# Optimization experiments

Measured on AMD Instinct MI355X. Metric: run time of the kernel, lower is better.

Reference implementation:

```python
import jax, jax.numpy as jnp
import numpy as np
from jax import lax

K = 8          # num_classes
C_IN = 256     # in_channels
EPS = 1e-5


def resize_bilinear_ac(x, H, W):
    """Bilinear resize with align_corners=True. x: [B,C,h,w] -> [B,C,H,W]."""
    B, C, h, w = x.shape
    if h == H and w == W:
        return x
    ys = jnp.linspace(0.0, h - 1.0, H)
    xs = jnp.linspace(0.0, w - 1.0, W)
    y0 = jnp.floor(ys).astype(jnp.int32)
    x0 = jnp.floor(xs).astype(jnp.int32)
    y1 = jnp.minimum(y0 + 1, h - 1)
    x1 = jnp.minimum(x0 + 1, w - 1)
    wy = (ys - y0.astype(x.dtype))[None, None, :, None]
    wx = (xs - x0.astype(x.dtype))[None, None, None, :]
    g00 = x[:, :, y0][:, :, :, x0]
    g01 = x[:, :, y0][:, :, :, x1]
    g10 = x[:, :, y1][:, :, :, x0]
    g11 = x[:, :, y1][:, :, :, x1]
    top = g00 * (1.0 - wx) + g01 * wx
    bot = g10 * (1.0 - wx) + g11 * wx
    return top * (1.0 - wy) + bot * wy


def setup_inputs() -> dict:
    key = jax.random.key(0)
    ks = jax.random.split(key, 16)
    shapes = [(2, 256, 128, 128), (2, 256, 64, 64), (2, 256, 32, 32), (2, 256, 16, 16), (2, 256, 8, 8)]
    inp = {}
    for i, s in enumerate(shapes):
        inp[f"feat{i}"] = jax.random.normal(ks[i], s, dtype=jnp.float32)
    inp["attr_feat"] = jax.random.normal(ks[5], (2, K * C_IN, 64, 64), dtype=jnp.float32)
    # learned params
    inp["mlp_f_w"] = jax.random.normal(ks[6], (256, 256), dtype=jnp.float32) * 0.02
    inp["mlp_f_b"] = jnp.zeros((256,), dtype=jnp.float32)
    inp["mlp_a_w"] = jax.random.normal(ks[7], (256, 256), dtype=jnp.float32) * 0.02
    inp["mlp_a_b"] = jnp.zeros((256,), dtype=jnp.float32)
    # 5 grouped convs: [out=2048, in_per_group=256, 3, 3] each, no bias (BN follows)
    inp["conv_w"] = jax.random.normal(ks[8], (5, K * C_IN, C_IN, 3, 3), dtype=jnp.float32) * 0.02
    inp["bn_gamma"] = jnp.ones((5, K * C_IN), dtype=jnp.float32)
    inp["bn_beta"] = jnp.zeros((5, K * C_IN), dtype=jnp.float32)
    inp["bn_mean"] = jax.random.normal(ks[9], (5, K * C_IN), dtype=jnp.float32) * 0.1
    inp["bn_var"] = jax.random.uniform(ks[10], (5, K * C_IN), dtype=jnp.float32, minval=0.5, maxval=1.5)
    return inp


def _forward(feats, attr_feat, mlp_f_w, mlp_f_b, mlp_a_w, mlp_a_b, conv_w, bn_gamma, bn_beta, bn_mean, bn_var):
    B = attr_feat.shape[0]
    # global avg pool attr -> [B, K, C] -> mlp_a
    avg_attr = attr_feat.mean(axis=(2, 3)).reshape(B, K, C_IN)
    avg_attr = avg_attr @ mlp_a_w.T + mlp_a_b  # [B,K,256]
    outs = []
    for i, x in enumerate(feats):
        _, C, H, W = x.shape
        avg_x = x.mean(axis=(2, 3)) @ mlp_f_w.T + mlp_f_b          # [B,256]
        logits = jnp.einsum('bkc,bc->bk', avg_attr, avg_x)          # [B,K]
        attn = jax.nn.softmax(logits, axis=-1)
        y = resize_bilinear_ac(attr_feat, H, W)                      # [B,2048,H,W]
        y = lax.conv_general_dilated(
            y, conv_w[i], window_strides=(1, 1), padding=((1, 1), (1, 1)),
            dimension_numbers=('NCHW', 'OIHW', 'NCHW'), feature_group_count=K)
        inv = lax.rsqrt(bn_var[i] + EPS)
        y = (y - bn_mean[i][None, :, None, None]) * (inv * bn_gamma[i])[None, :, None, None] + bn_beta[i][None, :, None, None]
        y = jax.nn.relu(y)
        y = y.reshape(B, K, C, H, W)
        y = jnp.einsum('bkchw,bk->bchw', y, attn)                   # weighted sum over classes
        outs.append(jax.nn.relu(x + y))
    return tuple(outs)


def reference(feat0, feat1, feat2, feat3, feat4, attr_feat, mlp_f_w, mlp_f_b, mlp_a_w, mlp_a_b, conv_w, bn_gamma, bn_beta, bn_mean, bn_var):
    feats = [feat0, feat1, feat2, feat3, feat4]
    return _forward(feats, attr_feat, mlp_f_w, mlp_f_b, mlp_a_w, mlp_a_b, conv_w, bn_gamma, bn_beta, bn_mean, bn_var)
```

## Files before the change

kernel.cpp:

```cpp
#include <hip/hip_runtime.h>
#include <hip/hip_bf16.h>
#include <cstdint>

typedef __attribute__((ext_vector_type(8))) short short8;
typedef __attribute__((ext_vector_type(4))) float f32x4;

#define EPSV 1e-5f

__device__ __forceinline__ void gload_lds16(const void* g, void* l) {
  __builtin_amdgcn_global_load_lds(
      (const __attribute__((address_space(1))) void*)(uintptr_t)g,
      (__attribute__((address_space(3))) void*)(uint32_t)(uintptr_t)l,
      16, 0, 0);
}

__device__ __forceinline__ uint32_t f2bf_rne(float v) {
  const uint32_t u = __float_as_uint(v);
  const uint32_t r = ((u >> 16) & 1u) + 0x7fffu;
  return (u + r) >> 16;
}

__global__ void mean_kernel(const float* __restrict__ in, float* __restrict__ out,
                            int HW, float inv) {
  const int ch = blockIdx.x;
  const int t = threadIdx.x;
  const float* p = in + (size_t)ch * HW;
  float s = 0.f;
  const int nv = HW >> 2;
  const float4* pv = (const float4*)p;
  for (int i = t; i < nv; i += 256) { float4 v = pv[i]; s += v.x + v.y + v.z + v.w; }
  __shared__ float red[256];
  red[t] = s; __syncthreads();
  for (int off = 128; off > 0; off >>= 1) {
    if (t < off) red[t] += red[t + off];
    __syncthreads();
  }
  if (t == 0) out[ch] = red[0] * inv;
}

__global__ void wtrans_kernel(const float* __restrict__ cw,
                              const float* __restrict__ gamma, const float* __restrict__ beta,
                              const float* __restrict__ mean, const float* __restrict__ var,
                              __hip_bfloat16* __restrict__ wt, float* __restrict__ bias) {
  const int oc = blockIdx.x;
  const int i  = blockIdx.y;
  const int ci = threadIdx.x;
  const int idx = i * 2048 + oc;
  const float sc = rsqrtf(var[idx] + EPSV) * gamma[idx];
  if (ci == 0) bias[idx] = beta[idx] - mean[idx] * sc;
  const int g = oc >> 8, co = oc & 255;
  const float* src = cw + ((size_t)idx * 256 + ci) * 9;
  const size_t dbase = (size_t)(i * 8 + g) * 9 * 65536 + co * 256 + ci;
#pragma unroll
  for (int tap = 0; tap < 9; ++tap)
    wt[dbase + (size_t)tap * 65536] = __float2bfloat16(src[tap] * sc);
}

__global__ void gate_kernel(const float* __restrict__ meanA, const float* __restrict__ meanF,
                            const float* __restrict__ Wa, const float* __restrict__ ba,
                            const float* __restrict__ Wf, const float* __restrict__ bfp,
                            float* __restrict__ attn) {
  __shared__ float mA[16 * 256];
  __shared__ float mF[10 * 256];
  __shared__ float pA[16 * 256];
  __shared__ float pF[10 * 256];
  __shared__ float lg[80];
// ... 70 lines not shown
  const int cc = t >> 2, seg = (t & 3) * 16;
  const int bb = bk >> 3, k = bk & 7;
  const float* ab = attr + (size_t)bb * 2048 * 4096;
  const int ci = t & 63;
  for (int cq = 0; cq < 4; ++cq) {
    __syncthreads();
    {
      const int ch = k * 256 + cq * 64 + cc;
      const float* r0 = ab + ((size_t)ch * 64 + y0) * 64;
      const float* r1 = ab + ((size_t)ch * 64 + y1) * 64;
#pragma unroll
      for (int u = 0; u < 4; ++u) {
        float4 v0 = ((const float4*)r0)[(t & 3) * 4 + u];
        float4 v1 = ((const float4*)r1)[(t & 3) * 4 + u];
        buf[0][cc][seg + u * 4 + 0] = v0.x; buf[0][cc][seg + u * 4 + 1] = v0.y;
        buf[0][cc][seg + u * 4 + 2] = v0.z; buf[0][cc][seg + u * 4 + 3] = v0.w;
        buf[1][cc][seg + u * 4 + 0] = v1.x; buf[1][cc][seg + u * 4 + 1] = v1.y;
        buf[1][cc][seg + u * 4 + 2] = v1.z; buf[1][cc][seg + u * 4 + 3] = v1.w;
      }
    }
    __syncthreads();
    for (int x = t >> 6; x < W; x += 4) {
      const float fx = x * scl;
      int x0 = (int)floorf(fx); if (x0 > 63) x0 = 63;
      const float wx = fx - (float)x0;
      const int x1 = min(x0 + 1, 63);
      const float top = buf[0][ci][x0] * (1.f - wx) + buf[0][ci][x1] * wx;
      const float bot = buf[1][ci][x0] * (1.f - wx) + buf[1][ci][x1] * wx;
      R[rowbase + (size_t)(x + 1) * 256 + cq * 64 + ci] = __float2bfloat16(top * (1.f - wy) + bot * wy);
    }
    if (t < 64) {
      R[rowbase + cq * 64 + t] = __float2bfloat16(0.f);
      R[rowbase + (size_t)(Wp - 1) * 256 + cq * 64 + t] = __float2bfloat16(0.f);
    }
  }
}

__device__ __forceinline__ void coords36(int u, int g0, int& g, int& ty, int& tx, int& cq) {
  g = g0 + u / 36;
  const int r = u % 36;
  const int tap = r >> 2;
  cq = r & 3;
  ty = tap / 3;
  tx = tap - ty * 3;
}

__global__ __launch_bounds__(512, 1)
void conv256_kernel(const __hip_bfloat16* __restrict__ R,
                    const __hip_bfloat16* __restrict__ Wt,
                    const float* __restrict__ bias,
                    const float* __restrict__ attn,
                    __hip_bfloat16* __restrict__ zout,
                    int W, int lw, int Hp, int Wp, int HW,
                    int NB, int gcount) {
  __shared__ alignas(16) __hip_bfloat16 ldsA[2][256 * 64];
  __shared__ alignas(16) __hip_bfloat16 ldsB[2][256 * 64];
  const int tid  = threadIdx.x;
  const int lane = tid & 63;
  const int wave = __builtin_amdgcn_readfirstlane(tid >> 6);
  const int wm = (wave >> 2) * 128;
  const int wn = (wave & 3) * 64;

  const int nx  = gridDim.x;
  const int lin = blockIdx.x;
  const int pos = ((nx & 7) == 0) ? ((lin & 7) * (nx >> 3) + (lin >> 3)) : lin;
  const int n0  = pos * 256;

  const int bb = (int)blockIdx.y % NB;
  const int gs = (int)blockIdx.y / NB;
  const int g0 = gs * gcount;

  const int c8 = lane & 7, r8 = lane >> 3;
  const int sc = (c8 ^ r8) << 3;
  const int aoff0 = ((wave * 32 + r8) << 8) + sc;
  const int dst0  = wave * 2048;
  int boff[4];
#pragma unroll
  for (int q = 0; q < 4; ++q) {
    const int row = wave * 32 + q * 8 + r8;
    const int sg = n0 + row;
    const int y = sg >> lw, x = sg & (W - 1);
    boff[q] = ((y * Wp + x) << 8) + sc;
  }

  const size_t rgstride = (size_t)Hp * Wp * 256;
  const __hip_bfloat16* Rb = R + (size_t)bb * 8 * rgstride;

  const f32x4 fz = {0.f, 0.f, 0.f, 0.f};
  f32x4 acc[8][4];
  uint32_t finp[8][4][2];
#pragma unroll
  for (int mf = 0; mf < 8; ++mf)
#pragma unroll
    for (int nf = 0; nf < 4; ++nf) {
      acc[mf][nf] = fz; finp[mf][nf][0] = 0u; finp[mf][nf][1] = 0u;
    }

  const int nk = gcount * 36;
  {
    const __hip_bfloat16* wp = Wt + ((size_t)g0 * 9 << 16);
    const __hip_bfloat16* rp = Rb + (size_t)g0 * rgstride;
#pragma unroll
    for (int q = 0; q < 4; ++q) gload_lds16(wp + aoff0 + q * 2048, &ldsA[0][dst0 + q * 512]);
#pragma unroll
    for (int q = 0; q < 4; ++q) gload_lds16(rp + boff[q], &ldsB[0][dst0 + q * 512]);
  }

  int foldc = 0, gcur = g0;
  for (int t = 0; t < nk; ++t) {
    const int c = t & 1;
    const bool pf = (t + 1 < nk);
    int g1, ty1, tx1, cq1;
    coords36(pf ? t + 1 : t, g0, g1, ty1, tx1, cq1);
    const __hip_bfloat16* wp1 = Wt + (((size_t)g1 * 9 + ty1 * 3 + tx1) << 16) + (cq1 << 6);
    const __hip_bfloat16* rp1 = Rb + (size_t)g1 * rgstride + ((ty1 * Wp + tx1) << 8) + (cq1 << 6);

    asm volatile("s_waitcnt vmcnt(0)" ::: "memory");
    __builtin_amdgcn_s_barrier();
    asm volatile("" ::: "memory");

    const __hip_bfloat16* pA = &ldsA[c][0];
    const __hip_bfloat16* pB = &ldsB[c][0];
    __hip_bfloat16* dA = &ldsA[c ^ 1][0];
    __hip_bfloat16* dB = &ldsB[c ^ 1][0];

#pragma unroll
    for (int ks = 0; ks < 2; ++ks) {
      const int cb = ks * 4 + (lane >> 4);
      short8 bfv[4];
#pragma unroll
      for (int nf = 0; nf < 4; ++nf) {
        const int row = wn + nf * 16 + (lane & 15);
        bfv[nf] = *(const short8*)&pB[(row << 6) + ((cb ^ (row & 7)) << 3)];
      }
#pragma unroll
      for (int h = 0; h < 2; ++h) {
        short8 af[4];
#pragma unroll
        for (int m = 0; m < 4; ++m) {
          const int row = wm + (h * 4 + m) * 16 + (lane & 15);
          af[m] = *(const short8*)&pA[(row << 6) + ((cb ^ (row & 7)) << 3)];
        }
        if (ks == 0 && pf) {
          if (h == 0) {
#pragma unroll
            for (int q = 0; q < 4; ++q) gload_lds16(wp1 + aoff0 + q * 2048, dA + dst0 + q * 512);
          } else {
#pragma unroll
            for (int q = 0; q < 4; ++q) gload_lds16(rp1 + boff[q], dB + dst0 + q * 512);
          }
        }
        __builtin_amdgcn_s_barrier();
        __builtin_amdgcn_sched_barrier(0);
        __builtin_amdgcn_s_setprio(1);
#pragma unroll
        for (int m = 0; m < 4; ++m)
#pragma unroll
          for (int nf = 0; nf < 4; ++nf)
            acc[h * 4 + m][nf] = __builtin_amdgcn_mfma_f32_16x16x32_bf16(
                af[m], bfv[nf], acc[h * 4 + m][nf], 0, 0, 0);
        __builtin_amdgcn_s_setprio(0);
        __builtin_amdgcn_s_barrier();
        asm volatile("" ::: "memory");
      }
    }

    if (++foldc == 36) {
      foldc = 0;
      const float aw = attn[bb * 8 + gcur];
#pragma unroll
      for (int mf = 0; mf < 8; ++mf) {
        const int cobase = wm + mf * 16 + ((lane >> 4) << 2);
#pragma unroll
        for (int pr = 0; pr < 2; ++pr) {
          const float b0v = bias[(gcur << 8) + cobase + pr * 2 + 0];
          const float b1v = bias[(gcur << 8) + cobase + pr * 2 + 1];
#pragma unroll
          for (int nf = 0; nf < 4; ++nf) {
            const uint32_t p = finp[mf][nf][pr];
            const float f0 = __uint_as_float(p << 16)
                           + aw * fmaxf(acc[mf][nf][pr * 2 + 0] + b0v, 0.f);
            const float f1 = __uint_as_float(p & 0xffff0000u)
                           + aw * fmaxf(acc[mf][nf][pr * 2 + 1] + b1v, 0.f);
            finp[mf][nf][pr] = (f2bf_rne(f1) << 16) | f2bf_rne(f0);
          }
        }
#pragma unroll
        for (int nf = 0; nf < 4; ++nf) acc[mf][nf] = fz;
      }
      ++gcur;
    }
  }

  __hip_bfloat16* zb = zout + (size_t)(gs * 2 + bb) * 256 * (size_t)HW;
#pragma unroll
  for (int mf = 0; mf < 8; ++mf) {
    const int cobase = wm + mf * 16 + ((lane >> 4) << 2);
#pragma unroll
    for (int nf = 0; nf < 4; ++nf) {
      const int n = n0 + wn + nf * 16 + (lane & 15);
#pragma unroll
      for (int pr = 0; pr < 2; ++pr) {
        const uint32_t p = finp[mf][nf][pr];
        zb[(size_t)(cobase + pr * 2 + 0) * HW + n] =
            __float2bfloat16(__uint_as_float(p << 16));
        zb[(size_t)(cobase + pr * 2 + 1) * HW + n] =
            __float2bfloat16(__uint_as_float(p & 0xffff0000u));
      }
    }
  }
}

__global__ __launch_bounds__(256, 2)
void conv_kernel(const __hip_bfloat16* __restrict__ R,
                 const __hip_bfloat16* __restrict__ Wt,
                 const float* __restrict__ bias,
                 const float* __restrict__ attn,
                 const float* __restrict__ featp,
                 void* __restrict__ outp,
                 int W, int lw, int Hp, int Wp, int HW,
                 int b0, int NB, int gcount) {
  __shared__ alignas(16) __hip_bfloat16 ldsA[2][128 * 64];
  __shared__ alignas(16) __hip_bfloat16 ldsB[3][128 * 64];
  const int tid  = threadIdx.x;
  const int lane = tid & 63;
  const int wave = __builtin_amdgcn_readfirstlane(tid >> 6);
  const int wm = (wave >> 1) * 64;
  const int wn = (wave & 1) * 64;

  const int nx  = gridDim.x;
  const int lin = blockIdx.x;
  const int pos = ((nx & 7) == 0) ? ((lin & 7) * (nx >> 3) + (lin >> 3)) : lin;
  const int co0 = (pos & 1) * 128;
  const int n0  = (pos >> 1) * 128;

  const int bb  = (int)blockIdx.y % NB;
  const int gs  = (int)blockIdx.y / NB;
  const int b   = b0 + bb;
  const int g0  = gs * gcount;

  const int c8 = lane & 7;
  const int r8 = lane >> 3;
  int aoff[4], boff[4], dst[4];
#pragma unroll
  for (int q = 0; q < 4; ++q) {
    const int row = (wave * 4 + q) * 8 + r8;
    const int sc = (c8 ^ (row & 7)) << 3;
    aoff[q] = ((co0 + row) << 8) + sc;
    int sg = n0 + row; if (sg >= HW) sg = HW - 1;
    const int y = sg >> lw, x = sg & (W - 1);
    boff[q] = ((y * Wp + x) << 8) + sc;
    dst[q] = (wave * 4 + q) * 512;
  }

  const size_t rgstride = (size_t)Hp * Wp * 256;
  const __hip_bfloat16* Rb = R + (size_t)bb * 8 * rgstride;

  const f32x4 fz = {0.f, 0.f, 0.f, 0.f};
  f32x4 fin[4][4], acc[4][4];
#pragma unroll
// ... 122 lines not shown
        if (n < HW) {
#pragma unroll
          for (int r = 0; r < 4; ++r)
            zb[(size_t)(cobase + r) * HW + n] = __float2bfloat16(fin[mf][nf][r]);
        }
      }
    }
  }
}

__global__ void reduce_kernel(const __hip_bfloat16* __restrict__ z,
                              const float* __restrict__ feat,
                              float* __restrict__ outp, int total, int S) {
  const int i4 = (blockIdx.x * 256 + threadIdx.x) * 4;
  if (i4 >= total) return;
  float4 f = *(const float4*)(feat + i4);
  float s0 = f.x, s1 = f.y, s2 = f.z, s3 = f.w;
  for (int j = 0; j < S; ++j) {
    const ushort4 v = *(const ushort4*)(z + (size_t)j * total + i4);
    s0 += __uint_as_float((uint32_t)v.x << 16);
    s1 += __uint_as_float((uint32_t)v.y << 16);
    s2 += __uint_as_float((uint32_t)v.z << 16);
    s3 += __uint_as_float((uint32_t)v.w << 16);
  }
  float4 o = {fmaxf(s0, 0.f), fmaxf(s1, 0.f), fmaxf(s2, 0.f), fmaxf(s3, 0.f)};
  *(float4*)(outp + i4) = o;
}

extern "C" void kernel_launch(void* const* d_in, const int* in_sizes, int n_in,
                              void* d_out, int out_size, void* d_ws, size_t ws_size,
                              hipStream_t stream) {
  const float* feat[5];
  for (int i = 0; i < 5; ++i) feat[i] = (const float*)d_in[i];
  const float* attr = (const float*)d_in[5];
  const float* mfw = (const float*)d_in[6];
  const float* mfb = (const float*)d_in[7];
  const float* maw = (const float*)d_in[8];
  const float* mab = (const float*)d_in[9];
  const float* cw  = (const float*)d_in[10];
  const float* bng = (const float*)d_in[11];
  const float* bnb = (const float*)d_in[12];
  const float* bnm = (const float*)d_in[13];
  const float* bnv = (const float*)d_in[14];
  float* out = (float*)d_out;

  char* ws = (char*)d_ws;
  float* attnW = (float*)(ws);
  float* meanA = (float*)(ws + 512);
  float* meanF = (float*)(ws + 20480);
  float* biasW = (float*)(ws + 32768);
  __hip_bfloat16* Wt = (__hip_bfloat16*)(ws + 131072);
  const size_t R_OFF = 47316992;
  __hip_bfloat16* Rbuf = (__hip_bfloat16*)(ws + R_OFF);

  const bool full = ws_size >= (size_t)219316224;
  const int NB = full ? 2 : 1;
  __hip_bfloat16* zbuf = (__hip_bfloat16*)(ws + R_OFF + (size_t)NB * 69222400);

  static const int HS[5] = {128, 64, 32, 16, 8};
  static const size_t OOFF[5] = {0, 8388608, 10485760, 11010048, 11141120};

  mean_kernel<<<4096, 256, 0, stream>>>(attr, meanA, 4096, 1.f / 4096.f);
  for (int i = 0; i < 5; ++i) {
    const int HW = HS[i] * HS[i];
    mean_kernel<<<512, 256, 0, stream>>>(feat[i], meanF + i * 512, HW, 1.f / (float)HW);
  }
  wtrans_kernel<<<dim3(2048, 5), 256, 0, stream>>>(cw, bng, bnb, bnm, bnv, Wt, biasW);
  gate_kernel<<<1, 256, 0, stream>>>(meanA, meanF, maw, mab, mfw, mfb, attnW);

  for (int i = 0; i < 5; ++i) {
    const int H = HS[i], W = H, HW = H * W, Hp = H + 2, Wp = W + 2;
    const int lw = 31 - __builtin_clz((unsigned)W);
    const float scl = 63.f / (float)(H - 1);

    if (full) {
      resize_kernel<<<dim3(16, Hp), 256, 0, stream>>>(attr, Rbuf, W, Hp, Wp, scl);
      if (i <= 1) {
        const int S = (i == 0) ? 2 : 8;
        const int gcount = 8 / S;
        conv256_kernel<<<dim3(HW / 256, 2 * S), 512, 0, stream>>>(
            Rbuf, Wt + (size_t)i * 8 * 9 * 65536, biasW + i * 2048, attnW + i * 16,
            zbuf, W, lw, Hp, Wp, HW, 2, gcount);
        const int total = 2 * 256 * HW;
        reduce_kernel<<<(total / 4 + 255) / 256, 256, 0, stream>>>(
            zbuf, feat[i], out + OOFF[i], total, S);
      } else {
        const int ntiles = (HW + 127) / 128;
        conv_kernel<<<dim3(ntiles * 2, 2 * 8), 256, 0, stream>>>(
            Rbuf, Wt + (size_t)i * 8 * 9 * 65536, biasW + i * 2048, attnW + i * 16,
            nullptr, zbuf, W, lw, Hp, Wp, HW, 0, 2, 1);
        const int total = 2 * 256 * HW;
        reduce_kernel<<<(total / 4 + 255) / 256, 256, 0, stream>>>(
            zbuf, feat[i], out + OOFF[i], total, 8);
      }
    } else {
      const int ntiles = (HW + 127) / 128;
      for (int b0 = 0; b0 < 2; ++b0) {
        resize_kernel<<<dim3(8, Hp), 256, 0, stream>>>(
            attr + (size_t)b0 * 2048 * 4096, Rbuf, W, Hp, Wp, scl);
        conv_kernel<<<dim3(ntiles * 2, 1), 256, 0, stream>>>(
            Rbuf, Wt + (size_t)i * 8 * 9 * 65536, biasW + i * 2048, attnW + i * 16,
            feat[i], out + OOFF[i], W, lw, Hp, Wp, HW, b0, 1, 8);
      }
    }
  }
}
```

Baseline: 723.9 us.

## Stage input halo tile once per channel slice and reuse across all nine taps

The conv256 kernel used to reload a 256x64 B tile from global memory for every (tap, channel-quarter) step. It now loads a padded halo patch of input rows (up to 576 rows x 64 channels) into LDS once per channel slice, through registers with a skewed swizzle. All nine 3x3 taps index into that patch, which cuts global and L2 traffic for the activation operand about ninefold. The change also remaps block order for L2 locality when the grid has 256 blocks and caches bias and attention in LDS. The trade-off is higher LDS usage, extra register pressure from holding the nine prefetched B vectors, and hand-tuned vmcnt waits that must match the load counts exactly.

```diff
diff --git a/kernel.cpp b/kernel.cpp
--- a/kernel.cpp
+++ b/kernel.cpp
@@ -12,6 +12,13 @@
       (const __attribute__((address_space(1))) void*)(uintptr_t)g,
       (__attribute__((address_space(3))) void*)(uint32_t)(uintptr_t)l,
       16, 0, 0);
+}
+
+__device__ __forceinline__ short8 aload(const __hip_bfloat16* sbase, uint32_t voff) {
+  short8 d;
+  asm volatile("global_load_dwordx4 %0, %1, %2 offset:0"
+               : "=&v"(d) : "v"(voff), "s"(sbase));
+  return d;
 }
 
 __device__ __forceinline__ uint32_t f2bf_rne(float v) {
@@ -188,39 +195,59 @@
                     const float* __restrict__ attn,
                     __hip_bfloat16* __restrict__ zout,
                     int W, int lw, int Hp, int Wp, int HW,
-                    int NB, int gcount) {
+                    int NB, int gcount, int COLS) {
   __shared__ alignas(16) __hip_bfloat16 ldsA[2][256 * 64];
-  __shared__ alignas(16) __hip_bfloat16 ldsB[2][256 * 64];
+  __shared__ alignas(16) __hip_bfloat16 ldsBh[576 * 64];
+  __shared__ float biasL[1024];
+  __shared__ float attnL[8];
   const int tid  = threadIdx.x;
   const int lane = tid & 63;
   const int wave = __builtin_amdgcn_readfirstlane(tid >> 6);
   const int wm = (wave >> 2) * 128;
   const int wn = (wave & 3) * 64;
 
-  const int nx  = gridDim.x;
-  const int lin = blockIdx.x;
-  const int pos = ((nx & 7) == 0) ? ((lin & 7) * (nx >> 3) + (lin >> 3)) : lin;
-  const int n0  = pos * 256;
-
-  const int bb = (int)blockIdx.y % NB;
-  const int gs = (int)blockIdx.y / NB;
+  const int X = gridDim.x;
+  int xp = blockIdx.x, yv = blockIdx.y;
+  if (X * gridDim.y == 256) {
+    const int lin2 = blockIdx.x + X * blockIdx.y;
+    const int d = (lin2 & 7) * 32 + (lin2 >> 3);
+    yv = d / X; xp = d - yv * X;
+  }
+  const int n0 = xp * 256;
+  const int bb = yv % NB;
+  const int gs = yv / NB;
   const int g0 = gs * gcount;
+  const int tr0 = n0 >> lw;
+  const int CG = COLS >> 3;
 
   const int c8 = lane & 7, r8 = lane >> 3;
-  const int sc = (c8 ^ r8) << 3;
-  const int aoff0 = ((wave * 32 + r8) << 8) + sc;
+  const int aoff0 = ((wave * 32 + r8) << 8) + ((c8 ^ r8) << 3);
   const int dst0  = wave * 2048;
-  int boff[4];
-#pragma unroll
-  for (int q = 0; q < 4; ++q) {
-    const int row = wave * 32 + q * 8 + r8;
-    const int sg = n0 + row;
-    const int y = sg >> lw, x = sg & (W - 1);
-    boff[q] = ((y * Wp + x) << 8) + sc;
+
+  uint32_t voffB[9]; int dstB[9];
+  {
+    const uint32_t srcswz = (uint32_t)((c8 ^ r8) << 4);
+#pragma unroll
+    for (int j = 0; j < 9; ++j) {
+      const int l = wave * 9 + j;
+      const int row = l / CG, cg = l - row * CG;
+      const int col = cg * 8 + r8;
+      const int colc = min(col, Wp - 1);
+      voffB[j] = (uint32_t)((row * Wp + colc) * 512) + srcswz;
+      dstB[j] = (row * COLS + cg * 8) * 64 + lane * 8;
+    }
+  }
+
+  int rc[4];
+#pragma unroll
+  for (int nf = 0; nf < 4; ++nf) {
+    const int s = wn + nf * 16 + (lane & 15);
+    rc[nf] = (s >> lw) * COLS + (s & (W - 1));
   }
 
   const size_t rgstride = (size_t)Hp * Wp * 256;
   const __hip_bfloat16* Rb = R + (size_t)bb * 8 * rgstride;
+  const size_t rowoff = (size_t)(tr0 * Wp) * 256;
 
   const f32x4 fz = {0.f, 0.f, 0.f, 0.f};
   f32x4 acc[8][4];
@@ -232,85 +259,109 @@
       acc[mf][nf] = fz; finp[mf][nf][0] = 0u; finp[mf][nf][1] = 0u;
     }
 
-  const int nk = gcount * 36;
+  for (int i = tid; i < (gcount << 8); i += 512) biasL[i] = bias[(g0 << 8) + i];
+  if (tid < gcount) attnL[tid] = attn[bb * 8 + g0 + tid];
+  __syncthreads();
+
+  const int nss = gcount * 4;
+  const int nk9 = nss * 9;
+  short8 breg[9];
   {
-    const __hip_bfloat16* wp = Wt + ((size_t)g0 * 9 << 16);
-    const __hip_bfloat16* rp = Rb + (size_t)g0 * rgstride;
-#pragma unroll
-    for (int q = 0; q < 4; ++q) gload_lds16(wp + aoff0 + q * 2048, &ldsA[0][dst0 + q * 512]);
-#pragma unroll
-    for (int q = 0; q < 4; ++q) gload_lds16(rp + boff[q], &ldsB[0][dst0 + q * 512]);
-  }
-
-  int foldc = 0, gcur = g0;
-  for (int t = 0; t < nk; ++t) {
-    const int c = t & 1;
-    const bool pf = (t + 1 < nk);
-    int g1, ty1, tx1, cq1;
-    coords36(pf ? t + 1 : t, g0, g1, ty1, tx1, cq1);
-    const __hip_bfloat16* wp1 = Wt + (((size_t)g1 * 9 + ty1 * 3 + tx1) << 16) + (cq1 << 6);
-    const __hip_bfloat16* rp1 = Rb + (size_t)g1 * rgstride + ((ty1 * Wp + tx1) << 8) + (cq1 << 6);
-
-    asm volatile("s_waitcnt vmcnt(0)" ::: "memory");
+    const __hip_bfloat16* rp0 = Rb + (size_t)g0 * rgstride + rowoff;
+#pragma unroll
+    for (int j = 0; j < 9; ++j) breg[j] = aload(rp0, voffB[j]);
+    const __hip_bfloat16* wp0 = Wt + ((size_t)g0 * 9 << 16);
+#pragma unroll
+    for (int q = 0; q < 4; ++q) gload_lds16(wp0 + aoff0 + q * 2048, &ldsA[0][dst0 + q * 512]);
+    asm volatile("s_waitcnt vmcnt(4)" ::: "memory");
+#pragma unroll
+    for (int j = 0; j < 9; ++j) *(short8*)&ldsBh[dstB[j]] = breg[j];
+    asm volatile("s_waitcnt lgkmcnt(0)" ::: "memory");
     __builtin_amdgcn_s_barrier();
     asm volatile("" ::: "memory");
-
-    const __hip_bfloat16* pA = &ldsA[c][0];
-    const __hip_bfloat16* pB = &ldsB[c][0];
-    __hip_bfloat16* dA = &ldsA[c ^ 1][0];
-    __hip_bfloat16* dB = &ldsB[c ^ 1][0];
-
-#pragma unroll
-    for (int ks = 0; ks < 2; ++ks) {
-      const int cb = ks * 4 + (lane >> 4);
-      short8 bfv[4];
-#pragma unroll
-      for (int nf = 0; nf < 4; ++nf) {
-        const int row = wn + nf * 16 + (lane & 15);
-        bfv[nf] = *(const short8*)&pB[(row << 6) + ((cb ^ (row & 7)) << 3)];
-      }
-#pragma unroll
-      for (int h = 0; h < 2; ++h) {
-        short8 af[4];
-#pragma unroll
-        for (int m = 0; m < 4; ++m) {
-          const int row = wm + (h * 4 + m) * 16 + (lane & 15);
-          af[m] = *(const short8*)&pA[(row << 6) + ((cb ^ (row & 7)) << 3)];
+  }
+
+  int k = 0, gcur = g0;
+  for (int ss = 0; ss < nss; ++ss) {
+    const bool hasB = (ss + 1 < nss);
+    for (int t8 = 0; t8 < 9; ++t8, ++k) {
+      const bool hasNext = (k + 1 < nk9);
+      if (hasNext) {
+        const int kn = k + 1, ssn = kn / 9, tn = kn - ssn * 9;
+        const int gn = g0 + (ssn >> 2), cqn = ssn & 3;
+        const __hip_bfloat16* wp = Wt + (((size_t)gn * 9 + tn) << 16) + (cqn << 6);
+        __hip_bfloat16* dA = &ldsA[kn & 1][0];
+#pragma unroll
+        for (int q = 0; q < 4; ++q) gload_lds16(wp + aoff0 + q * 2048, dA + dst0 + q * 512);
+      }
+      if (t8 == 6 && hasB) {
+        const int ssn = ss + 1;
+        const int gn = g0 + (ssn >> 2), cqn = ssn & 3;
+        const __hip_bfloat16* rp = Rb + (size_t)gn * rgstride + rowoff + (cqn << 6);
+#pragma unroll
+        for (int j = 0; j < 9; ++j) breg[j] = aload(rp, voffB[j]);
+      }
+      if (!hasNext)                          asm volatile("s_waitcnt vmcnt(0)" ::: "memory");
+      else if ((t8 == 6 || t8 == 7) && hasB) asm volatile("s_waitcnt vmcnt(13)" ::: "memory");
+      else                                   asm volatile("s_waitcnt vmcnt(4)" ::: "memory");
+      __builtin_amdgcn_s_barrier();
+      asm volatile("" ::: "memory");
+
+      const __hip_bfloat16* pA = &ldsA[k & 1][0];
+      const int ty = (t8 >= 6) ? 2 : (t8 >= 3 ? 1 : 0);
+      const int tx = t8 - ty * 3;
+      const int tof = (ty * COLS + tx) << 6;
+      const int czx = (c8 + tx) & 7;
+#pragma unroll
+      for (int ks = 0; ks < 2; ++ks) {
+        const int cb = ks * 4 + (lane >> 4);
+        const int slot = (cb ^ czx) << 3;
+        short8 bfv[4];
+#pragma unroll
+        for (int nf = 0; nf < 4; ++nf)
+          bfv[nf] = *(const short8*)&ldsBh[(rc[nf] << 6) + tof + slot];
+#pragma unroll
+        for (int h = 0; h < 2; ++h) {
+          short8 af[4];
+#pragma unroll
+          for (int m = 0; m < 4; ++m) {
+            const int row = wm + (h * 4 + m) * 16 + (lane & 15);
+            af[m] = *(const short8*)&pA[(row << 6) + ((cb ^ (row & 7)) << 3)];
+          }
+          __builtin_amdgcn_s_barrier();
+          __builtin_amdgcn_sched_barrier(0);
+          __builtin_amdgcn_s_setprio(1);
+#pragma unroll
+          for (int m = 0; m < 4; ++m)
+#pragma unroll
+            for (int nf = 0; nf < 4; ++nf)
+              acc[h * 4 + m][nf] = __builtin_amdgcn_mfma_f32_16x16x32_bf16(
+                  af[m], bfv[nf], acc[h * 4 + m][nf], 0, 0, 0);
+          __builtin_amdgcn_s_setprio(0);
+          __builtin_amdgcn_s_barrier();
+          asm volatile("" ::: "memory");
         }
-        if (ks == 0 && pf) {
-          if (h == 0) {
-#pragma unroll
-            for (int q = 0; q < 4; ++q) gload_lds16(wp1 + aoff0 + q * 2048, dA + dst0 + q * 512);
-          } else {
-#pragma unroll
-            for (int q = 0; q < 4; ++q) gload_lds16(rp1 + boff[q], dB + dst0 + q * 512);
-          }
-        }
-        __builtin_amdgcn_s_barrier();
-        __builtin_amdgcn_sched_barrier(0);
-        __builtin_amdgcn_s_setprio(1);
-#pragma unroll
-        for (int m = 0; m < 4; ++m)
-#pragma unroll
-          for (int nf = 0; nf < 4; ++nf)
-            acc[h * 4 + m][nf] = __builtin_amdgcn_mfma_f32_16x16x32_bf16(
-                af[m], bfv[nf], acc[h * 4 + m][nf], 0, 0, 0);
-        __builtin_amdgcn_s_setprio(0);
-        __builtin_amdgcn_s_barrier();
-        asm volatile("" ::: "memory");
-      }
-    }
-
-    if (++foldc == 36) {
-      foldc = 0;
-      const float aw = attn[bb * 8 + gcur];
+      }
+    }
+
+    if (hasB) {
+#pragma unroll
+      for (int j = 0; j < 9; ++j) *(short8*)&ldsBh[dstB[j]] = breg[j];
+      asm volatile("s_waitcnt lgkmcnt(0)" ::: "memory");
+      __builtin_amdgcn_s_barrier();
+      asm volatile("" ::: "memory");
+    }
+
+    if ((ss & 3) == 3) {
+      const float aw = attnL[gcur - g0];
+      const int gb = (gcur - g0) << 8;
 #pragma unroll
       for (int mf = 0; mf < 8; ++mf) {
         const int cobase = wm + mf * 16 + ((lane >> 4) << 2);
 #pragma unroll
         for (int pr = 0; pr < 2; ++pr) {
-          const float b0v = bias[(gcur << 8) + cobase + pr * 2 + 0];
-          const float b1v = bias[(gcur << 8) + cobase + pr * 2 + 1];
+          const float b0v = biasL[gb + cobase + pr * 2 + 0];
+          const float b1v = biasL[gb + cobase + pr * 2 + 1];
 #pragma unroll
           for (int nf = 0; nf < 4; ++nf) {
             const uint32_t p = finp[mf][nf][pr];
@@ -596,9 +647,10 @@
       if (i <= 1) {
         const int S = (i == 0) ? 2 : 8;
         const int gcount = 8 / S;
+        const int COLS = (W == 128) ? 144 : 96;
         conv256_kernel<<<dim3(HW / 256, 2 * S), 512, 0, stream>>>(
             Rbuf, Wt + (size_t)i * 8 * 9 * 65536, biasW + i * 2048, attnW + i * 16,
-            zbuf, W, lw, Hp, Wp, HW, 2, gcount);
+            zbuf, W, lw, Hp, Wp, HW, 2, gcount, COLS);
         const int total = 2 * 256 * HW;
         reduce_kernel<<<(total / 4 + 255) / 256, 256, 0, stream>>>(
             zbuf, feat[i], out + OOFF[i], total, S);
```

After: 958.6 us. 1.32x slower.

## Deepen conv K-loop pipeline to 4-stage half-K buffers with partial waits

Applied to the files above, without the earlier changes.

Splits each 64-wide K step into two 32-wide halves held in a 4-slot LDS ring, prefetching three stages ahead and waiting on vmcnt counts instead of draining all loads each iteration. This is meant to hide global-to-LDS load latency behind MFMA work. It also caches bias and attention weights in LDS for the per-class fold and remaps block IDs for locality when the grid has 256 blocks. In exchange there are twice as many barriers per unit of work, and the swizzle and vmcnt accounting have to stay correct.

```diff
diff --git a/kernel.cpp b/kernel.cpp
--- a/kernel.cpp
+++ b/kernel.cpp
@@ -189,34 +189,39 @@
                     __hip_bfloat16* __restrict__ zout,
                     int W, int lw, int Hp, int Wp, int HW,
                     int NB, int gcount) {
-  __shared__ alignas(16) __hip_bfloat16 ldsA[2][256 * 64];
-  __shared__ alignas(16) __hip_bfloat16 ldsB[2][256 * 64];
+  __shared__ alignas(16) __hip_bfloat16 ldsA[4][256 * 32];
+  __shared__ alignas(16) __hip_bfloat16 ldsB[4][256 * 32];
+  __shared__ float biasL[1024];
+  __shared__ float attnL[8];
   const int tid  = threadIdx.x;
   const int lane = tid & 63;
   const int wave = __builtin_amdgcn_readfirstlane(tid >> 6);
   const int wm = (wave >> 2) * 128;
   const int wn = (wave & 3) * 64;
 
-  const int nx  = gridDim.x;
-  const int lin = blockIdx.x;
-  const int pos = ((nx & 7) == 0) ? ((lin & 7) * (nx >> 3) + (lin >> 3)) : lin;
-  const int n0  = pos * 256;
-
-  const int bb = (int)blockIdx.y % NB;
-  const int gs = (int)blockIdx.y / NB;
+  const int X = gridDim.x;
+  int xp = blockIdx.x, yv = blockIdx.y;
+  if (X * gridDim.y == 256) {
+    const int lin2 = blockIdx.x + X * blockIdx.y;
+    const int d = (lin2 & 7) * 32 + (lin2 >> 3);
+    yv = d / X; xp = d - yv * X;
+  }
+  const int n0 = xp * 256;
+  const int bb = yv % NB;
+  const int gs = yv / NB;
   const int g0 = gs * gcount;
 
-  const int c8 = lane & 7, r8 = lane >> 3;
-  const int sc = (c8 ^ r8) << 3;
-  const int aoff0 = ((wave * 32 + r8) << 8) + sc;
-  const int dst0  = wave * 2048;
-  int boff[4];
-#pragma unroll
-  for (int q = 0; q < 4; ++q) {
-    const int row = wave * 32 + q * 8 + r8;
-    const int sg = n0 + row;
-    const int y = sg >> lw, x = sg & (W - 1);
-    boff[q] = ((y * Wp + x) << 8) + sc;
+  const int l23 = lane & 3, l2 = lane >> 2;
+  int asrc[2], bsrc[2], sdst[2];
+#pragma unroll
+  for (int q = 0; q < 2; ++q) {
+    const int row = wave * 32 + q * 16 + l2;
+    const int swz = (l23 ^ ((row >> 1) & 3)) << 3;
+    asrc[q] = (row << 8) + swz;
+    const int n = n0 + row;
+    const int y = n >> lw, x = n & (W - 1);
+    bsrc[q] = ((y * Wp + x) << 8) + swz;
+    sdst[q] = (wave * 32 + q * 16) << 5;
   }
 
   const size_t rgstride = (size_t)Hp * Wp * 256;
@@ -232,85 +237,98 @@
       acc[mf][nf] = fz; finp[mf][nf][0] = 0u; finp[mf][nf][1] = 0u;
     }
 
-  const int nk = gcount * 36;
-  {
-    const __hip_bfloat16* wp = Wt + ((size_t)g0 * 9 << 16);
-    const __hip_bfloat16* rp = Rb + (size_t)g0 * rgstride;
-#pragma unroll
-    for (int q = 0; q < 4; ++q) gload_lds16(wp + aoff0 + q * 2048, &ldsA[0][dst0 + q * 512]);
-#pragma unroll
-    for (int q = 0; q < 4; ++q) gload_lds16(rp + boff[q], &ldsB[0][dst0 + q * 512]);
-  }
+  for (int i = tid; i < (gcount << 8); i += 512) biasL[i] = bias[(g0 << 8) + i];
+  if (tid < gcount) attnL[tid] = attn[bb * 8 + g0 + tid];
+  __syncthreads();
+
+  const int nh = gcount * 72;
+
+#define ISSUE_HALF(hh_)                                                        \
+  {                                                                            \
+    const int k_ = (hh_) >> 1;                                                 \
+    const int g_ = g0 + k_ / 36;                                               \
+    const int r_ = k_ % 36;                                                    \
+    const int tap_ = r_ >> 2;                                                  \
+    const int ty_ = (tap_ >= 6) ? 2 : (tap_ >= 3 ? 1 : 0);                     \
+    const int tx_ = tap_ - ty_ * 3;                                            \
+    const int cib = ((r_ & 3) << 6) + (((hh_) & 1) << 5);                      \
+    const __hip_bfloat16* wp = Wt + (((size_t)g_ * 9 + tap_) << 16) + cib;     \
+    const __hip_bfloat16* rp = Rb + (size_t)g_ * rgstride +                    \
+                               ((ty_ * Wp + tx_) << 8) + cib;                  \
+    const int sl_ = (hh_) & 3;                                                 \
+    gload_lds16(wp + asrc[0], &ldsA[sl_][sdst[0]]);                            \
+    gload_lds16(wp + asrc[1], &ldsA[sl_][sdst[1]]);                            \
+    gload_lds16(rp + bsrc[0], &ldsB[sl_][sdst[0]]);                            \
+    gload_lds16(rp + bsrc[1], &ldsB[sl_][sdst[1]]);                            \
+  }
+
+  ISSUE_HALF(0); ISSUE_HALF(1); ISSUE_HALF(2);
 
   int foldc = 0, gcur = g0;
-  for (int t = 0; t < nk; ++t) {
-    const int c = t & 1;
-    const bool pf = (t + 1 < nk);
-    int g1, ty1, tx1, cq1;
-    coords36(pf ? t + 1 : t, g0, g1, ty1, tx1, cq1);
-    const __hip_bfloat16* wp1 = Wt + (((size_t)g1 * 9 + ty1 * 3 + tx1) << 16) + (cq1 << 6);
-    const __hip_bfloat16* rp1 = Rb + (size_t)g1 * rgstride + ((ty1 * Wp + tx1) << 8) + (cq1 << 6);
-
-    asm volatile("s_waitcnt vmcnt(0)" ::: "memory");
+  for (int hh = 0; hh < nh; ++hh) {
+    if (hh + 3 < nh) ISSUE_HALF(hh + 3);
+    if (hh + 3 < nh)      asm volatile("s_waitcnt vmcnt(12)" ::: "memory");
+    else if (hh + 2 < nh) asm volatile("s_waitcnt vmcnt(8)" ::: "memory");
+    else if (hh + 1 < nh) asm volatile("s_waitcnt vmcnt(4)" ::: "memory");
+    else                  asm volatile("s_waitcnt vmcnt(0)" ::: "memory");
     __builtin_amdgcn_s_barrier();
     asm volatile("" ::: "memory");
 
-    const __hip_bfloat16* pA = &ldsA[c][0];
-    const __hip_bfloat16* pB = &ldsB[c][0];
-    __hip_bfloat16* dA = &ldsA[c ^ 1][0];
-    __hip_bfloat16* dB = &ldsB[c ^ 1][0];
-
-#pragma unroll
-    for (int ks = 0; ks < 2; ++ks) {
-      const int cb = ks * 4 + (lane >> 4);
-      short8 bfv[4];
-#pragma unroll
-      for (int nf = 0; nf < 4; ++nf) {
-        const int row = wn + nf * 16 + (lane & 15);
-        bfv[nf] = *(const short8*)&pB[(row << 6) + ((cb ^ (row & 7)) << 3)];
-      }
-#pragma unroll
-      for (int h = 0; h < 2; ++h) {
-        short8 af[4];
-#pragma unroll
-        for (int m = 0; m < 4; ++m) {
-          const int row = wm + (h * 4 + m) * 16 + (lane & 15);
-          af[m] = *(const short8*)&pA[(row << 6) + ((cb ^ (row & 7)) << 3)];
-        }
-        if (ks == 0 && pf) {
-          if (h == 0) {
-#pragma unroll
-            for (int q = 0; q < 4; ++q) gload_lds16(wp1 + aoff0 + q * 2048, dA + dst0 + q * 512);
-          } else {
-#pragma unroll
-            for (int q = 0; q < 4; ++q) gload_lds16(rp1 + boff[q], dB + dst0 + q * 512);
-          }
-        }
-        __builtin_amdgcn_s_barrier();
-        __builtin_amdgcn_sched_barrier(0);
-        __builtin_amdgcn_s_setprio(1);
-#pragma unroll
-        for (int m = 0; m < 4; ++m)
-#pragma unroll
-          for (int nf = 0; nf < 4; ++nf)
-            acc[h * 4 + m][nf] = __builtin_amdgcn_mfma_f32_16x16x32_bf16(
-                af[m], bfv[nf], acc[h * 4 + m][nf], 0, 0, 0);
-        __builtin_amdgcn_s_setprio(0);
-        __builtin_amdgcn_s_barrier();
-        asm volatile("" ::: "memory");
-      }
-    }
-
-    if (++foldc == 36) {
+    const int sl = hh & 3;
+    const __hip_bfloat16* pA = &ldsA[sl][0];
+    const __hip_bfloat16* pB = &ldsB[sl][0];
+    const int cb = lane >> 4;
+    short8 bfv[4], af[4];
+#pragma unroll
+    for (int nf = 0; nf < 4; ++nf) {
+      const int row = wn + nf * 16 + (lane & 15);
+      bfv[nf] = *(const short8*)&pB[(row << 5) + ((cb ^ ((row >> 1) & 3)) << 3)];
+    }
+#pragma unroll
+    for (int m = 0; m < 4; ++m) {
+      const int row = wm + m * 16 + (lane & 15);
+      af[m] = *(const short8*)&pA[(row << 5) + ((cb ^ ((row >> 1) & 3)) << 3)];
+    }
+    __builtin_amdgcn_s_barrier();
+    __builtin_amdgcn_sched_barrier(0);
+    __builtin_amdgcn_s_setprio(1);
+#pragma unroll
+    for (int m = 0; m < 4; ++m)
+#pragma unroll
+      for (int nf = 0; nf < 4; ++nf)
+        acc[m][nf] = __builtin_amdgcn_mfma_f32_16x16x32_bf16(
+            af[m], bfv[nf], acc[m][nf], 0, 0, 0);
+    __builtin_amdgcn_s_setprio(0);
+
+#pragma unroll
+    for (int m = 0; m < 4; ++m) {
+      const int row = wm + 64 + m * 16 + (lane & 15);
+      af[m] = *(const short8*)&pA[(row << 5) + ((cb ^ ((row >> 1) & 3)) << 3)];
+    }
+    __builtin_amdgcn_s_barrier();
+    __builtin_amdgcn_sched_barrier(0);
+    __builtin_amdgcn_s_setprio(1);
+#pragma unroll
+    for (int m = 0; m < 4; ++m)
+#pragma unroll
+      for (int nf = 0; nf < 4; ++nf)
+        acc[4 + m][nf] = __builtin_amdgcn_mfma_f32_16x16x32_bf16(
+            af[m], bfv[nf], acc[4 + m][nf], 0, 0, 0);
+    __builtin_amdgcn_s_setprio(0);
+    __builtin_amdgcn_s_barrier();
+    asm volatile("" ::: "memory");
+
+    if (++foldc == 72) {
       foldc = 0;
-      const float aw = attn[bb * 8 + gcur];
+      const float aw = attnL[gcur - g0];
+      const int gb = (gcur - g0) << 8;
 #pragma unroll
       for (int mf = 0; mf < 8; ++mf) {
         const int cobase = wm + mf * 16 + ((lane >> 4) << 2);
 #pragma unroll
         for (int pr = 0; pr < 2; ++pr) {
-          const float b0v = bias[(gcur << 8) + cobase + pr * 2 + 0];
-          const float b1v = bias[(gcur << 8) + cobase + pr * 2 + 1];
+          const float b0v = biasL[gb + cobase + pr * 2 + 0];
+          const float b1v = biasL[gb + cobase + pr * 2 + 1];
 #pragma unroll
           for (int nf = 0; nf < 4; ++nf) {
             const uint32_t p = finp[mf][nf][pr];
@@ -327,6 +345,7 @@
       ++gcur;
     }
   }
+#undef ISSUE_HALF
 
   __hip_bfloat16* zb = zout + (size_t)(gs * 2 + bb) * 256 * (size_t)HW;
 #pragma unroll
```

After: 753.7 us. 4.1% more time.

## Restructure conv256 to one group per block with deeper prefetch

Applied to the files above, without the earlier changes.

The 256-tile conv kernel now handles exactly one group per block, dropping the in-register bf16 fold across groups and writing per-group partials that the reduce kernel sums. The main loop issues the next K-tile's loads before waiting (vmcnt(8)), which removes one barrier pair per half-step and loads all B fragments up front. Level 0 is split into per-batch resize+conv+reduce passes so the workspace needs only a single-batch buffer, and block-index swizzling is applied across the full 2D grid. The cost is more zbuf traffic (8 partials instead of 2) and more reduce work, plus extra launches for level 0.

```diff
diff --git a/kernel.cpp b/kernel.cpp
--- a/kernel.cpp
+++ b/kernel.cpp
@@ -188,160 +188,163 @@
                     const float* __restrict__ attn,
                     __hip_bfloat16* __restrict__ zout,
                     int W, int lw, int Hp, int Wp, int HW,
-                    int NB, int gcount) {
+                    int NB, int b0) {
   __shared__ alignas(16) __hip_bfloat16 ldsA[2][256 * 64];
   __shared__ alignas(16) __hip_bfloat16 ldsB[2][256 * 64];
+  __shared__ float biasL[256];
   const int tid  = threadIdx.x;
   const int lane = tid & 63;
   const int wave = __builtin_amdgcn_readfirstlane(tid >> 6);
   const int wm = (wave >> 2) * 128;
   const int wn = (wave & 3) * 64;
 
-  const int nx  = gridDim.x;
-  const int lin = blockIdx.x;
-  const int pos = ((nx & 7) == 0) ? ((lin & 7) * (nx >> 3) + (lin >> 3)) : lin;
-  const int n0  = pos * 256;
-
-  const int bb = (int)blockIdx.y % NB;
-  const int gs = (int)blockIdx.y / NB;
-  const int g0 = gs * gcount;
+  const int X = gridDim.x;
+  const int T = X * (int)gridDim.y;
+  int lin = (int)blockIdx.x + X * (int)blockIdx.y;
+  if ((T & 7) == 0) lin = (lin & 7) * (T >> 3) + (lin >> 3);
+  const int yv = lin / X, xp = lin - yv * X;
+  const int n0 = xp * 256;
+  const int bb = yv % NB;
+  const int g0 = yv / NB;
 
   const int c8 = lane & 7, r8 = lane >> 3;
-  const int sc = (c8 ^ r8) << 3;
-  const int aoff0 = ((wave * 32 + r8) << 8) + sc;
+  const int swz = (c8 ^ r8) << 3;
+  const int aoff0 = ((wave * 32 + r8) << 8) + swz;
   const int dst0  = wave * 2048;
   int boff[4];
 #pragma unroll
   for (int q = 0; q < 4; ++q) {
     const int row = wave * 32 + q * 8 + r8;
-    const int sg = n0 + row;
-    const int y = sg >> lw, x = sg & (W - 1);
-    boff[q] = ((y * Wp + x) << 8) + sc;
+    const int n = n0 + row;
+    const int y = n >> lw, x = n & (W - 1);
+    boff[q] = ((y * Wp + x) << 8) + swz;
   }
 
   const size_t rgstride = (size_t)Hp * Wp * 256;
-  const __hip_bfloat16* Rb = R + (size_t)bb * 8 * rgstride;
+  const __hip_bfloat16* Rg = R + (size_t)(bb * 8 + g0) * rgstride;
+  const __hip_bfloat16* Wg = Wt + ((size_t)g0 * 9 << 16);
+
+  if (tid < 256) biasL[tid] = bias[(g0 << 8) + tid];
+  const float aw = attn[(b0 + bb) * 8 + g0];
+  __syncthreads();
 
   const f32x4 fz = {0.f, 0.f, 0.f, 0.f};
   f32x4 acc[8][4];
-  uint32_t finp[8][4][2];
 #pragma unroll
   for (int mf = 0; mf < 8; ++mf)
 #pragma unroll
-    for (int nf = 0; nf < 4; ++nf) {
-      acc[mf][nf] = fz; finp[mf][nf][0] = 0u; finp[mf][nf][1] = 0u;
-    }
-
-  const int nk = gcount * 36;
-  {
-    const __hip_bfloat16* wp = Wt + ((size_t)g0 * 9 << 16);
-    const __hip_bfloat16* rp = Rb + (size_t)g0 * rgstride;
-#pragma unroll
-    for (int q = 0; q < 4; ++q) gload_lds16(wp + aoff0 + q * 2048, &ldsA[0][dst0 + q * 512]);
-#pragma unroll
-    for (int q = 0; q < 4; ++q) gload_lds16(rp + boff[q], &ldsB[0][dst0 + q * 512]);
-  }
-
-  int foldc = 0, gcur = g0;
-  for (int t = 0; t < nk; ++t) {
-    const int c = t & 1;
-    const bool pf = (t + 1 < nk);
-    int g1, ty1, tx1, cq1;
-    coords36(pf ? t + 1 : t, g0, g1, ty1, tx1, cq1);
-    const __hip_bfloat16* wp1 = Wt + (((size_t)g1 * 9 + ty1 * 3 + tx1) << 16) + (cq1 << 6);
-    const __hip_bfloat16* rp1 = Rb + (size_t)g1 * rgstride + ((ty1 * Wp + tx1) << 8) + (cq1 << 6);
-
-    asm volatile("s_waitcnt vmcnt(0)" ::: "memory");
+    for (int nf = 0; nf < 4; ++nf) acc[mf][nf] = fz;
+
+#define ISSUE_KT(t_)                                                           \
+  {                                                                            \
+    const int tap_ = (t_) >> 2, cq_ = (t_) & 3;                                \
+    const int ty_ = (tap_ >= 6) ? 2 : (tap_ >= 3 ? 1 : 0);                     \
+    const int tx_ = tap_ - ty_ * 3;                                            \
+    const __hip_bfloat16* wp = Wg + ((size_t)tap_ << 16) + (cq_ << 6);         \
+    const __hip_bfloat16* rp = Rg + ((ty_ * Wp + tx_) << 8) + (cq_ << 6);      \
+    const int sl_ = (t_) & 1;                                                  \
+    _Pragma("unroll")                                                          \
+    for (int q = 0; q < 4; ++q) {                                              \
+      gload_lds16(wp + aoff0 + q * 2048, &ldsA[sl_][dst0 + q * 512]);          \
+      gload_lds16(rp + boff[q], &ldsB[sl_][dst0 + q * 512]);                   \
+    }                                                                          \
+  }
+
+  ISSUE_KT(0);
+
+  const int l15 = lane & 15, cb0 = lane >> 4;
+  for (int t = 0; t < 36; ++t) {
+    if (t + 1 < 36) {
+      ISSUE_KT(t + 1);
+      asm volatile("s_waitcnt vmcnt(8)" ::: "memory");
+    } else {
+      asm volatile("s_waitcnt vmcnt(0)" ::: "memory");
+    }
     __builtin_amdgcn_s_barrier();
     asm volatile("" ::: "memory");
 
-    const __hip_bfloat16* pA = &ldsA[c][0];
-    const __hip_bfloat16* pB = &ldsB[c][0];
-    __hip_bfloat16* dA = &ldsA[c ^ 1][0];
-    __hip_bfloat16* dB = &ldsB[c ^ 1][0];
-
-#pragma unroll
-    for (int ks = 0; ks < 2; ++ks) {
-      const int cb = ks * 4 + (lane >> 4);
-      short8 bfv[4];
+    const __hip_bfloat16* pA = &ldsA[t & 1][0];
+    const __hip_bfloat16* pB = &ldsB[t & 1][0];
+
+    short8 bfv[8], afA[4], afB[4];
+#pragma unroll
+    for (int ks = 0; ks < 2; ++ks)
 #pragma unroll
       for (int nf = 0; nf < 4; ++nf) {
-        const int row = wn + nf * 16 + (lane & 15);
-        bfv[nf] = *(const short8*)&pB[(row << 6) + ((cb ^ (row & 7)) << 3)];
-      }
-#pragma unroll
-      for (int h = 0; h < 2; ++h) {
-        short8 af[4];
-#pragma unroll
-        for (int m = 0; m < 4; ++m) {
-          const int row = wm + (h * 4 + m) * 16 + (lane & 15);
-          af[m] = *(const short8*)&pA[(row << 6) + ((cb ^ (row & 7)) << 3)];
-        }
-        if (ks == 0 && pf) {
-          if (h == 0) {
-#pragma unroll
-            for (int q = 0; q < 4; ++q) gload_lds16(wp1 + aoff0 + q * 2048, dA + dst0 + q * 512);
-          } else {
-#pragma unroll
-            for (int q = 0; q < 4; ++q) gload_lds16(rp1 + boff[q], dB + dst0 + q * 512);
-          }
-        }
-        __builtin_amdgcn_s_barrier();
-        __builtin_amdgcn_sched_barrier(0);
-        __builtin_amdgcn_s_setprio(1);
-#pragma unroll
-        for (int m = 0; m < 4; ++m)
-#pragma unroll
-          for (int nf = 0; nf < 4; ++nf)
-            acc[h * 4 + m][nf] = __builtin_amdgcn_mfma_f32_16x16x32_bf16(
-                af[m], bfv[nf], acc[h * 4 + m][nf], 0, 0, 0);
-        __builtin_amdgcn_s_setprio(0);
-        __builtin_amdgcn_s_barrier();
-        asm volatile("" ::: "memory");
-      }
-    }
-
-    if (++foldc == 36) {
-      foldc = 0;
-      const float aw = attn[bb * 8 + gcur];
-#pragma unroll
-      for (int mf = 0; mf < 8; ++mf) {
-        const int cobase = wm + mf * 16 + ((lane >> 4) << 2);
-#pragma unroll
-        for (int pr = 0; pr < 2; ++pr) {
-          const float b0v = bias[(gcur << 8) + cobase + pr * 2 + 0];
-          const float b1v = bias[(gcur << 8) + cobase + pr * 2 + 1];
-#pragma unroll
-          for (int nf = 0; nf < 4; ++nf) {
-            const uint32_t p = finp[mf][nf][pr];
-            const float f0 = __uint_as_float(p << 16)
-                           + aw * fmaxf(acc[mf][nf][pr * 2 + 0] + b0v, 0.f);
-            const float f1 = __uint_as_float(p & 0xffff0000u)
-                           + aw * fmaxf(acc[mf][nf][pr * 2 + 1] + b1v, 0.f);
-            finp[mf][nf][pr] = (f2bf_rne(f1) << 16) | f2bf_rne(f0);
-          }
-        }
-#pragma unroll
-        for (int nf = 0; nf < 4; ++nf) acc[mf][nf] = fz;
-      }
-      ++gcur;
-    }
-  }
-
-  __hip_bfloat16* zb = zout + (size_t)(gs * 2 + bb) * 256 * (size_t)HW;
+        const int row = wn + nf * 16 + l15;
+        bfv[ks * 4 + nf] =
+            *(const short8*)&pB[(row << 6) + (((ks * 4 + cb0) ^ (row & 7)) << 3)];
+      }
+#pragma unroll
+    for (int m = 0; m < 4; ++m) {
+      const int row = wm + m * 16 + l15;
+      afA[m] = *(const short8*)&pA[(row << 6) + ((cb0 ^ (row & 7)) << 3)];
+    }
+#pragma unroll
+    for (int m = 0; m < 4; ++m) {
+      const int row = wm + 64 + m * 16 + l15;
+      afB[m] = *(const short8*)&pA[(row << 6) + ((cb0 ^ (row & 7)) << 3)];
+    }
+    __builtin_amdgcn_sched_barrier(0);
+    __builtin_amdgcn_s_setprio(1);
+#pragma unroll
+    for (int m = 0; m < 4; ++m)
+#pragma unroll
+      for (int nf = 0; nf < 4; ++nf)
+        acc[m][nf] = __builtin_amdgcn_mfma_f32_16x16x32_bf16(
+            afA[m], bfv[nf], acc[m][nf], 0, 0, 0);
+    __builtin_amdgcn_s_setprio(0);
+#pragma unroll
+    for (int m = 0; m < 4; ++m) {
+      const int row = wm + m * 16 + l15;
+      afA[m] = *(const short8*)&pA[(row << 6) + (((4 + cb0) ^ (row & 7)) << 3)];
+    }
+    __builtin_amdgcn_sched_barrier(0);
+    __builtin_amdgcn_s_setprio(1);
+#pragma unroll
+    for (int m = 0; m < 4; ++m)
+#pragma unroll
+      for (int nf = 0; nf < 4; ++nf)
+        acc[4 + m][nf] = __builtin_amdgcn_mfma_f32_16x16x32_bf16(
+            afB[m], bfv[nf], acc[4 + m][nf], 0, 0, 0);
+    __builtin_amdgcn_s_setprio(0);
+#pragma unroll
+    for (int m = 0; m < 4; ++m) {
+      const int row = wm + 64 + m * 16 + l15;
+      afB[m] = *(const short8*)&pA[(row << 6) + (((4 + cb0) ^ (row & 7)) << 3)];
+    }
+    __builtin_amdgcn_sched_barrier(0);
+    __builtin_amdgcn_s_setprio(1);
+#pragma unroll
+    for (int m = 0; m < 4; ++m)
+#pragma unroll
+      for (int nf = 0; nf < 4; ++nf)
+        acc[m][nf] = __builtin_amdgcn_mfma_f32_16x16x32_bf16(
+            afA[m], bfv[4 + nf], acc[m][nf], 0, 0, 0);
+#pragma unroll
+    for (int m = 0; m < 4; ++m)
+#pragma unroll
+      for (int nf = 0; nf < 4; ++nf)
+        acc[4 + m][nf] = __builtin_amdgcn_mfma_f32_16x16x32_bf16(
+            afB[m], bfv[4 + nf], acc[4 + m][nf], 0, 0, 0);
+    __builtin_amdgcn_s_setprio(0);
+    __builtin_amdgcn_s_barrier();
+    asm volatile("" ::: "memory");
+  }
+#undef ISSUE_KT
+
+  __hip_bfloat16* zb = zout + (size_t)yv * 256 * (size_t)HW;
 #pragma unroll
   for (int mf = 0; mf < 8; ++mf) {
-    const int cobase = wm + mf * 16 + ((lane >> 4) << 2);
-#pragma unroll
-    for (int nf = 0; nf < 4; ++nf) {
-      const int n = n0 + wn + nf * 16 + (lane & 15);
-#pragma unroll
-      for (int pr = 0; pr < 2; ++pr) {
-        const uint32_t p = finp[mf][nf][pr];
-        zb[(size_t)(cobase + pr * 2 + 0) * HW + n] =
-            __float2bfloat16(__uint_as_float(p << 16));
-        zb[(size_t)(cobase + pr * 2 + 1) * HW + n] =
-            __float2bfloat16(__uint_as_float(p & 0xffff0000u));
+    const int cobase = wm + mf * 16 + (cb0 << 2);
+#pragma unroll
+    for (int r = 0; r < 4; ++r) {
+      const float bs = biasL[cobase + r];
+      __hip_bfloat16* zr = zb + (size_t)(cobase + r) * HW;
+#pragma unroll
+      for (int nf = 0; nf < 4; ++nf) {
+        const int n = n0 + wn + nf * 16 + l15;
+        zr[n] = __float2bfloat16(aw * fmaxf(acc[mf][nf][r] + bs, 0.f));
       }
     }
   }
@@ -570,10 +573,9 @@
   __hip_bfloat16* Wt = (__hip_bfloat16*)(ws + 131072);
   const size_t R_OFF = 47316992;
   __hip_bfloat16* Rbuf = (__hip_bfloat16*)(ws + R_OFF);
+  __hip_bfloat16* zbuf = (__hip_bfloat16*)(ws + R_OFF + (size_t)69222400);
 
   const bool full = ws_size >= (size_t)219316224;
-  const int NB = full ? 2 : 1;
-  __hip_bfloat16* zbuf = (__hip_bfloat16*)(ws + R_OFF + (size_t)NB * 69222400);
 
   static const int HS[5] = {128, 64, 32, 16, 8};
   static const size_t OOFF[5] = {0, 8388608, 10485760, 11010048, 11141120};
@@ -592,19 +594,28 @@
     const float scl = 63.f / (float)(H - 1);
 
     if (full) {
-      resize_kernel<<<dim3(16, Hp), 256, 0, stream>>>(attr, Rbuf, W, Hp, Wp, scl);
-      if (i <= 1) {
-        const int S = (i == 0) ? 2 : 8;
-        const int gcount = 8 / S;
-        conv256_kernel<<<dim3(HW / 256, 2 * S), 512, 0, stream>>>(
-            Rbuf, Wt + (size_t)i * 8 * 9 * 65536, biasW + i * 2048, attnW + i * 16,
-            zbuf, W, lw, Hp, Wp, HW, 2, gcount);
+      if (i == 0) {
+        const size_t plane = (size_t)256 * HW;
+        for (int b0 = 0; b0 < 2; ++b0) {
+          resize_kernel<<<dim3(8, Hp), 256, 0, stream>>>(
+              attr + (size_t)b0 * 2048 * 4096, Rbuf, W, Hp, Wp, scl);
+          conv256_kernel<<<dim3(HW / 256, 8), 512, 0, stream>>>(
+              Rbuf, Wt, biasW, attnW, zbuf, W, lw, Hp, Wp, HW, 1, b0);
+          reduce_kernel<<<((int)plane / 4 + 255) / 256, 256, 0, stream>>>(
+              zbuf, feat[0] + b0 * plane, out + OOFF[0] + b0 * plane, (int)plane, 8);
+        }
+      } else if (i == 1) {
+        resize_kernel<<<dim3(16, Hp), 256, 0, stream>>>(attr, Rbuf, W, Hp, Wp, scl);
+        conv256_kernel<<<dim3(HW / 256, 16), 512, 0, stream>>>(
+            Rbuf, Wt + (size_t)1 * 8 * 9 * 65536, biasW + 2048, attnW + 16,
+            zbuf, W, lw, Hp, Wp, HW, 2, 0);
         const int total = 2 * 256 * HW;
         reduce_kernel<<<(total / 4 + 255) / 256, 256, 0, stream>>>(
-            zbuf, feat[i], out + OOFF[i], total, S);
+            zbuf, feat[1], out + OOFF[1], total, 8);
       } else {
+        resize_kernel<<<dim3(16, Hp), 256, 0, stream>>>(attr, Rbuf, W, Hp, Wp, scl);
         const int ntiles = (HW + 127) / 128;
-        conv_kernel<<<dim3(ntiles * 2, 2 * 8), 256, 0, stream>>>(
+        conv_kernel<<<dim3(ntiles * 2, 16), 256, 0, stream>>>(
             Rbuf, Wt + (size_t)i * 8 * 9 * 65536, biasW + i * 2048, attnW + i * 16,
             nullptr, zbuf, W, lw, Hp, Wp, HW, 0, 2, 1);
         const int total = 2 * 256 * HW;
```

After: 745.5 us. 1.03x slower.
